# Performance work log

Hardware: AMD Instinct MI355X
Metric: run time of the kernel (lower is better)

The kernel has to match this reference:

```python
import jax, jax.numpy as jnp
import numpy as np
import math

D_MODEL = 512
N_HEADS = 8
D_HEAD = D_MODEL // N_HEADS
TEMP = math.sqrt(D_HEAD)


def setup_inputs() -> dict:
    key = jax.random.key(0)
    k1, k2, k3, k4, k5, k6 = jax.random.split(key, 6)
    B, L = 4, 2048
    q = jax.random.normal(k1, (B, L, D_MODEL), dtype=jnp.float32)
    # bool mask, True -> zero out post-softmax attention (matches torch.where branch)
    mask = jax.random.bernoulli(k2, 0.1, (B, L, L))
    in_weight = jax.random.normal(k3, (3 * D_MODEL, D_MODEL), dtype=jnp.float32) * 0.02
    in_bias = jax.random.normal(k4, (3 * D_MODEL,), dtype=jnp.float32) * 0.02
    out_w = jax.random.normal(k5, (D_MODEL, D_MODEL), dtype=jnp.float32) * 0.02
    out_b = jax.random.normal(k6, (D_MODEL,), dtype=jnp.float32) * 0.02
    return {"q": q, "mask": mask, "in_weight": in_weight, "in_bias": in_bias,
            "out_w": out_w, "out_b": out_b}


def reference(q, mask, in_weight, in_bias, out_w, out_b):
    B, L, D = q.shape
    # per-head weight slicing exactly as the torch reshape: (H, E, 3, D)
    W = in_weight.reshape(N_HEADS, D_HEAD, 3, D)
    Bv = in_bias.reshape(N_HEADS, D_HEAD, 3)
    qw, kw, vw = W[:, :, 0, :], W[:, :, 1, :], W[:, :, 2, :]  # (H, E, D)
    qb, kb, vb = Bv[:, :, 0], Bv[:, :, 1], Bv[:, :, 2]        # (H, E)
    # self-attention: k = q, v = q (forward defaults)
    Q = jnp.einsum('bld,hed->bhle', q, qw) + qb[None, :, None, :]
    K = jnp.einsum('bld,hed->bhle', q, kw) + kb[None, :, None, :]
    V = jnp.einsum('bld,hed->bhle', q, vw) + vb[None, :, None, :]
    atn = jax.nn.softmax(jnp.einsum('bhqe,bhke->bhqk', Q, K) / TEMP, axis=-1)
    # post-softmax bool masking (faithful to the original non-standard order)
    atn = jnp.where(mask[:, None, :, :], jnp.zeros((), atn.dtype), atn)
    # QUIRK of source: attention() returns V (not atn @ V); heads = concat of V
    heads = V.transpose(0, 2, 1, 3).reshape(B, L, D)  # (B, L, D_MODEL)
    outputs = heads @ out_w.T + out_b
    masks = atn.sum(axis=1)  # sum over heads -> (B, Lq, Lk)
    return outputs, masks
```

## Files before the change

kernel.cpp:

```cpp
#include <hip/hip_runtime.h>

typedef unsigned short u16;
typedef unsigned int u32;
typedef __bf16 bf16x8 __attribute__((ext_vector_type(8)));
typedef float f32x4 __attribute__((ext_vector_type(4)));

#define B_SZ 4
#define L_SZ 2048
#define D_SZ 512
#define H_SZ 8
#define E_SZ 64

#define Q_SCALE 0.18033688011112042f

#define WS_FLAG   0
#define WS_WPACK  1024
#define WS_BPACK  (WS_WPACK + 1572864)
#define WS_WOUT   (WS_BPACK + 6144)
#define WS_QBF    (WS_WOUT + 524288)
#define WS_Q      (WS_QBF + 8388608)
#define WS_K      (WS_Q + 8388608)
#define WS_V      (WS_K + 8388608)
#define WS_STATS  (WS_V + 8388608)

static __device__ __forceinline__ u16 f2bf(float f) {
  unsigned int u = __float_as_uint(f);
  u += 0x7FFFu + ((u >> 16) & 1u);
  return (u16)(u >> 16);
}

static __device__ __forceinline__ float fexp2(float x) {
  return __builtin_amdgcn_exp2f(x);
}

union FragU { bf16x8 v; uint4 u4; unsigned long long ul[2]; };

static __device__ __forceinline__ int gperm(int d) {
  int t = d & 31;
  return (d & ~31) | ((t & 12) << 1) | ((t & 16) >> 2) | (t & 3);
}

static __device__ __forceinline__ bf16x8 qfrag(const u16* __restrict__ Qp,
                                               int row, int half, int lg) {
  FragU f;
  f.u4 = *reinterpret_cast<const uint4*>(
      (const char*)Qp + (size_t)row * 128 + (half << 6) + (lg << 4));
  return f.v;
}

static __device__ __forceinline__ void gload_lds16(const void* g, void* l) {
  __builtin_amdgcn_global_load_lds(
      (const __attribute__((address_space(1))) void*)g,
      (__attribute__((address_space(3))) void*)l, 16, 0, 0);
}

static __device__ __forceinline__ void stage_k128(const u16* __restrict__ Kh, int kb0,
                                                  char* tile, int w, int lane) {
#pragma unroll
  for (int i = 0; i < 4; i++) {
    int r = w * 32 + i * 8 + (lane >> 3);
    int y = (lane & 7) << 4;
    const char* g = (const char*)Kh + (size_t)(kb0 + r) * 128 + (y ^ ((r & 7) << 4));
    gload_lds16(g, tile + w * 4096 + i * 1024);
  }
}

static __device__ __forceinline__ bf16x8 lds_frag(const char* tile, int c, int half,
                                                  int lr, int lg) {
  int r = c * 16 + lr;
  int off = ((half << 6) | (lg << 4)) ^ ((r & 7) << 4);
  FragU f;
  f.u4 = *reinterpret_cast<const uint4*>(tile + r * 128 + off);
  return f.v;
}

__global__ __launch_bounds__(256) void kdetect(const unsigned int* __restrict__ w,
                                               int* __restrict__ flag) {
  int fB = 0, fF = 0;
  for (int i = blockIdx.x * blockDim.x + threadIdx.x; i < 262144;
       i += gridDim.x * blockDim.x) {
    unsigned int v = w[i];
    if (v == 0x3F800000u) fF = 1;
    else if (v > 1u) fB = 1;
  }
  if (__any(fB)) { if ((threadIdx.x & 63) == 0) atomicOr(&flag[0], 1); }
  if (__any(fF)) { if ((threadIdx.x & 63) == 0) atomicOr(&flag[1], 1); }
}

__global__ __launch_bounds__(256) void kcast(const float* __restrict__ q,
                                             u16* __restrict__ qbf) {
  int i = blockIdx.x * blockDim.x + threadIdx.x;
  int row = i >> 6, c = i & 63;
  int g = c >> 2, lg = c & 3;
  const float* src = q + (size_t)row * 512 + g * 32 + lg * 4;
  float4 v0 = *reinterpret_cast<const float4*>(src);
  float4 v1 = *reinterpret_cast<const float4*>(src + 16);
  u32 w0 = f2bf(v0.x) | ((u32)f2bf(v0.y) << 16);
  u32 w1 = f2bf(v0.z) | ((u32)f2bf(v0.w) << 16);
  u32 w2 = f2bf(v1.x) | ((u32)f2bf(v1.y) << 16);
  u32 w3 = f2bf(v1.z) | ((u32)f2bf(v1.w) << 16);
  uint4 out = {w0, w1, w2, w3};
  *reinterpret_cast<uint4*>(qbf + (size_t)row * 512 + c * 8) = out;
}

__global__ __launch_bounds__(256) void kpack(const float* __restrict__ w_in,
                                             const float* __restrict__ b_in,
                                             const float* __restrict__ w_out,
                                             u16* __restrict__ Wpack, float* __restrict__ bpack,
                                             u16* __restrict__ Wout) {
  const int T0 = 1536 * 512;
  const int T1 = T0 + 512 * 512;
  const int T2 = T1 + 1536;
  for (int i = blockIdx.x * blockDim.x + threadIdx.x; i < T2; i += gridDim.x * blockDim.x) {
    if (i < T0) {
      int n = i >> 9, d = i & 511;
      int sel = n >> 9, idx = n & 511;
      int h = idx >> 6, e = idx & 63;
      int row = h * 192 + e * 3 + sel;
      float v = w_in[row * 512 + d];
      if (sel == 0) v *= Q_SCALE;
      Wpack[(size_t)n * 512 + gperm(d)] = f2bf(v);
    } else if (i < T1) {
      int j = i - T0;
      int n = j >> 9, d = j & 511;
      Wout[(size_t)n * 512 + gperm(d)] = f2bf(w_out[j]);
    } else {
      int n = i - T1;
      int sel = n >> 9, idx = n & 511;
      int h = idx >> 6, e = idx & 63;
      int row = h * 192 + e * 3 + sel;
      float v = b_in[row];
      if (sel == 0) v *= Q_SCALE;
      bpack[n] = v;
    }
  }
}

static __device__ __forceinline__ void stage_tile(const u16* __restrict__ A,
                                                  const u16* __restrict__ Bw,
                                                  int m0, int n0, int t,
                                                  char* tA, char* tB, int tid) {
  int w64 = tid & ~63;
#pragma unroll
  for (int i = 0; i < 4; i++) {
    int cl = tid + i * 256;
    int r = cl >> 3, c = cl & 7;
    size_t gofs = (size_t)r * 1024 + t * 128 + ((c ^ (r & 7)) << 4);
    gload_lds16((const char*)A + (size_t)m0 * 1024 + gofs, tA + (i * 256 + w64) * 16);
    gload_lds16((const char*)Bw + (size_t)n0 * 1024 + gofs, tB + (i * 256 + w64) * 16);
  }
}

template<int MODE>
__global__ __launch_bounds__(256) void kgemm(const u16* __restrict__ A,
                                             const u16* __restrict__ Bw,
                                             const float* __restrict__ bias,
                                             u16* __restrict__ Qb, u16* __restrict__ Kb,
                                             u16* __restrict__ Vb, float* __restrict__ outp) {
  __shared__ __align__(128) char tA[2][16384], tB[2][16384];
  int tid = threadIdx.x;
  int w = tid >> 6, lane = tid & 63;
  int lr = lane & 15, lg = lane >> 4;
  int m0 = blockIdx.x * 128, n0 = blockIdx.y * 128;
  int wr = w >> 1, wc = w & 1;

  f32x4 acc[4][4] = {};

  stage_tile(A, Bw, m0, n0, 0, tA[0], tB[0], tid);
  __syncthreads();
#pragma unroll 1
  for (int t = 0; t < 8; t++) {
    if (t < 7) stage_tile(A, Bw, m0, n0, t + 1, tA[(t + 1) & 1], tB[(t + 1) & 1], tid);
    const char* mA = tA[t & 1] + wr * 64 * 128;
    const char* mB = tB[t & 1] + wc * 64 * 128;
#pragma unroll
    for (int gg = 0; gg < 2; gg++) {
      bf16x8 af[4], bf_[4];
#pragma unroll
      for (int i = 0; i < 4; i++) af[i] = lds_frag(mA, i, gg, lr, lg);
#pragma unroll
      for (int j = 0; j < 4; j++) bf_[j] = lds_frag(mB, j, gg, lr, lg);
#pragma unroll
      for (int i = 0; i < 4; i++)
#pragma unroll
        for (int j = 0; j < 4; j++)
          acc[i][j] = __builtin_amdgcn_mfma_f32_16x16x32_bf16(af[i], bf_[j], acc[i][j], 0, 0, 0);
    }
    __syncthreads();
  }

#pragma unroll
  for (int j = 0; j < 4; j++) {
    int col = n0 + wc * 64 + j * 16 + lr;
    float bb = bias[col];
#pragma unroll
    for (int i = 0; i < 4; i++) {
#pragma unroll
      for (int jj = 0; jj < 4; jj++) {
        int row = m0 + wr * 64 + i * 16 + lg * 4 + jj;
        float val = acc[i][j][jj] + bb;
        if (MODE == 1) {
          outp[(size_t)row * 512 + col] = val;
        } else {
          u16 bv = f2bf(val);
          int b = row >> 11, l = row & 2047;
          if (col < 512) {
            int h = col >> 6, e = col & 63;
            Qb[((((size_t)(b * 8 + h)) << 11) + l) * 64 + gperm(e)] = bv;
          } else if (col < 1024) {
            int c2 = col - 512, h = c2 >> 6, e = c2 & 63;
            Kb[((((size_t)(b * 8 + h)) << 11) + l) * 64 + gperm(e)] = bv;
          } else {
            Vb[(size_t)row * 512 + gperm(col - 1024)] = bv;
          }
        }
      }
    }
  }
}

__global__ __launch_bounds__(256, 4) void kstats(const u16* __restrict__ Qb,
                                                 const u16* __restrict__ Kb,
                                                 float* __restrict__ stats) {
  __shared__ __align__(128) char tile[2][16384];
  int bh = blockIdx.x;
  int w = threadIdx.x >> 6, lane = threadIdx.x & 63;
  int lr = lane & 15, lg = lane >> 4;
  int q0 = blockIdx.y * 64 + w * 16;
  const u16* Qp = Qb + (size_t)bh * L_SZ * E_SZ;
  const u16* Kp = Kb + (size_t)bh * L_SZ * E_SZ;

  bf16x8 bq0 = qfrag(Qp, q0 + lr, 0, lg);
  bf16x8 bq1 = qfrag(Qp, q0 + lr, 1, lg);
  float s = 0.0f;

  stage_k128(Kp, 0, tile[0], w, lane);
  __syncthreads();
#pragma unroll 1
  for (int t = 0; t < 16; t++) {
    if (t + 1 < 16) stage_k128(Kp, (t + 1) * 128, tile[(t + 1) & 1], w, lane);
    const char* tl = tile[t & 1];
#pragma unroll 2
    for (int c = 0; c < 8; c++) {
      bf16x8 a0 = lds_frag(tl, c, 0, lr, lg);
      bf16x8 a1 = lds_frag(tl, c, 1, lr, lg);
      f32x4 d = {0.f, 0.f, 0.f, 0.f};
      d = __builtin_amdgcn_mfma_f32_16x16x32_bf16(a0, bq0, d, 0, 0, 0);
      d = __builtin_amdgcn_mfma_f32_16x16x32_bf16(a1, bq1, d, 0, 0, 0);
      s += fexp2(d[0]) + fexp2(d[1]) + fexp2(d[2]) + fexp2(d[3]);
    }
    __syncthreads();
  }
  s += __shfl_xor(s, 16);
  s += __shfl_xor(s, 32);
  if (lane < 16) stats[(size_t)bh * L_SZ + q0 + lr] = 1.0f / s;
}

__global__ __launch_bounds__(256, 4) void kmasks(const u16* __restrict__ Qb,
                                                 const u16* __restrict__ Kb,
                                                 const float* __restrict__ stats,
                                                 const void* __restrict__ mask,
                                                 const int* __restrict__ flag,
                                                 float* __restrict__ outp) {
  __shared__ __align__(128) char tile[2][16384];
  int b = blockIdx.z;
  int w = threadIdx.x >> 6, lane = threadIdx.x & 63;
  int lr = lane & 15, lg = lane >> 4;
  int q0 = blockIdx.y * 64 + w * 16;
  int kb0 = blockIdx.x * 128;
  int mode = flag[0] ? 1 : (flag[1] ? 2 : 0);

  f32x4 P[8] = {};

  stage_k128(Kb + (size_t)(b * 8) * L_SZ * E_SZ, kb0, tile[0], w, lane);
  __syncthreads();
#pragma unroll 1
  for (int h = 0; h < 8; h++) {
    if (h + 1 < 8)
      stage_k128(Kb + (size_t)(b * 8 + h + 1) * L_SZ * E_SZ, kb0, tile[(h + 1) & 1], w, lane);
    const u16* Qp = Qb + (size_t)(b * 8 + h) * L_SZ * E_SZ;
    bf16x8 bq0 = qfrag(Qp, q0 + lr, 0, lg);
    bf16x8 bq1 = qfrag(Qp, q0 + lr, 1, lg);
    float rr = stats[(size_t)(b * 8 + h) * L_SZ + q0 + lr];
    const char* tl = tile[h & 1];
#pragma unroll 2
    for (int c = 0; c < 8; c++) {
      bf16x8 a0 = lds_frag(tl, c, 0, lr, lg);
      bf16x8 a1 = lds_frag(tl, c, 1, lr, lg);
      f32x4 d = {0.f, 0.f, 0.f, 0.f};
      d = __builtin_amdgcn_mfma_f32_16x16x32_bf16(a0, bq0, d, 0, 0, 0);
      d = __builtin_amdgcn_mfma_f32_16x16x32_bf16(a1, bq1, d, 0, 0, 0);
#pragma unroll
      for (int j = 0; j < 4; j++) P[c][j] += fexp2(d[j]) * rr;
    }
    __syncthreads();
  }

  int q = q0 + lr;
  float* mrow = outp + (size_t)B_SZ * L_SZ * D_SZ
              + (size_t)b * L_SZ * L_SZ + (size_t)q * L_SZ + kb0;
  size_t moff = (size_t)b * L_SZ * L_SZ + (size_t)q * L_SZ + kb0;
#pragma unroll
  for (int c = 0; c < 8; c++) {
    int kk = c * 16 + lg * 4;
    f32x4 v = P[c];
    if (mode == 1) {
      u32 mb = *reinterpret_cast<const u32*>((const unsigned char*)mask + moff + kk);
      if ((mb      ) & 0xFF) v[0] = 0.f;
      if ((mb >>  8) & 0xFF) v[1] = 0.f;
      if ((mb >> 16) & 0xFF) v[2] = 0.f;
      if ((mb >> 24) & 0xFF) v[3] = 0.f;
    } else if (mode == 0) {
      int4 mi = *reinterpret_cast<const int4*>((const int*)mask + moff + kk);
      if (mi.x) v[0] = 0.f;
      if (mi.y) v[1] = 0.f;
      if (mi.z) v[2] = 0.f;
      if (mi.w) v[3] = 0.f;
    } else {
      float4 mf = *reinterpret_cast<const float4*>((const float*)mask + moff + kk);
      if (mf.x != 0.f) v[0] = 0.f;
      if (mf.y != 0.f) v[1] = 0.f;
      if (mf.z != 0.f) v[2] = 0.f;
      if (mf.w != 0.f) v[3] = 0.f;
    }
    *reinterpret_cast<f32x4*>(mrow + kk) = v;
  }
}

extern "C" void kernel_launch(void* const* d_in, const int* in_sizes, int n_in,
                              void* d_out, int out_size, void* d_ws, size_t ws_size,
                              hipStream_t stream) {
  (void)in_sizes; (void)n_in; (void)out_size; (void)ws_size;
  const float* q     = (const float*)d_in[0];
  const void*  mask  = d_in[1];
  const float* w_in  = (const float*)d_in[2];
  const float* b_in  = (const float*)d_in[3];
  const float* w_out = (const float*)d_in[4];
  const float* b_out = (const float*)d_in[5];
  float* outp = (float*)d_out;
  char* ws = (char*)d_ws;

  int*    flag  = (int*)(ws + WS_FLAG);
  u16*    Wpack = (u16*)(ws + WS_WPACK);
  float*  bpack = (float*)(ws + WS_BPACK);
  u16*    Wout  = (u16*)(ws + WS_WOUT);
  u16*    qbf   = (u16*)(ws + WS_QBF);
  u16*    Qb    = (u16*)(ws + WS_Q);
  u16*    Kb    = (u16*)(ws + WS_K);
  u16*    Vb    = (u16*)(ws + WS_V);
  float*  stats = (float*)(ws + WS_STATS);

  hipMemsetAsync(flag, 0, 16, stream);
  hipLaunchKernelGGL(kdetect, dim3(256), dim3(256), 0, stream, (const unsigned int*)mask, flag);
  hipLaunchKernelGGL(kcast, dim3(2048), dim3(256), 0, stream, q, qbf);
  hipLaunchKernelGGL(kpack, dim3(2048), dim3(256), 0, stream, w_in, b_in, w_out,
                     Wpack, bpack, Wout);
  hipLaunchKernelGGL((kgemm<0>), dim3(64, 12), dim3(256), 0, stream,
                     qbf, Wpack, bpack, Qb, Kb, Vb, (float*)nullptr);
  hipLaunchKernelGGL((kgemm<1>), dim3(64, 4), dim3(256), 0, stream,
                     Vb, Wout, b_out, (u16*)nullptr, (u16*)nullptr, (u16*)nullptr, outp);
  hipLaunchKernelGGL(kstats, dim3(32, 32), dim3(256), 0, stream, Qb, Kb, stats);
  hipLaunchKernelGGL(kmasks, dim3(16, 32, 4), dim3(256), 0, stream, Qb, Kb, stats, mask, flag, outp);
}
```

Measured before the change: 148.3 us.

## Load K fragments directly from global memory instead of LDS staging

Drops the double-buffered LDS staging of K tiles in both the stats and masks kernels. Each wave now reads its K fragments straight from global memory, relying on L1/L2 to serve the reuse across waves. This removes the barriers and the LDS footprint, which may raise occupancy. The masks kernel also prefetches the next head's Q fragments and row statistic into registers. The cost is redundant global and cache traffic, since four waves read the same K rows, and less control over latency hiding.

```diff
diff --git a/kernel.cpp b/kernel.cpp
--- a/kernel.cpp
+++ b/kernel.cpp
@@ -52,17 +52,6 @@
   __builtin_amdgcn_global_load_lds(
       (const __attribute__((address_space(1))) void*)g,
       (__attribute__((address_space(3))) void*)l, 16, 0, 0);
-}
-
-static __device__ __forceinline__ void stage_k128(const u16* __restrict__ Kh, int kb0,
-                                                  char* tile, int w, int lane) {
-#pragma unroll
-  for (int i = 0; i < 4; i++) {
-    int r = w * 32 + i * 8 + (lane >> 3);
-    int y = (lane & 7) << 4;
-    const char* g = (const char*)Kh + (size_t)(kb0 + r) * 128 + (y ^ ((r & 7) << 4));
-    gload_lds16(g, tile + w * 4096 + i * 1024);
-  }
 }
 
 static __device__ __forceinline__ bf16x8 lds_frag(const char* tile, int c, int half,
@@ -222,7 +211,6 @@
 __global__ __launch_bounds__(256, 4) void kstats(const u16* __restrict__ Qb,
                                                  const u16* __restrict__ Kb,
                                                  float* __restrict__ stats) {
-  __shared__ __align__(128) char tile[2][16384];
   int bh = blockIdx.x;
   int w = threadIdx.x >> 6, lane = threadIdx.x & 63;
   int lr = lane & 15, lg = lane >> 4;
@@ -234,22 +222,14 @@
   bf16x8 bq1 = qfrag(Qp, q0 + lr, 1, lg);
   float s = 0.0f;
 
-  stage_k128(Kp, 0, tile[0], w, lane);
-  __syncthreads();
-#pragma unroll 1
-  for (int t = 0; t < 16; t++) {
-    if (t + 1 < 16) stage_k128(Kp, (t + 1) * 128, tile[(t + 1) & 1], w, lane);
-    const char* tl = tile[t & 1];
-#pragma unroll 2
-    for (int c = 0; c < 8; c++) {
-      bf16x8 a0 = lds_frag(tl, c, 0, lr, lg);
-      bf16x8 a1 = lds_frag(tl, c, 1, lr, lg);
-      f32x4 d = {0.f, 0.f, 0.f, 0.f};
-      d = __builtin_amdgcn_mfma_f32_16x16x32_bf16(a0, bq0, d, 0, 0, 0);
-      d = __builtin_amdgcn_mfma_f32_16x16x32_bf16(a1, bq1, d, 0, 0, 0);
-      s += fexp2(d[0]) + fexp2(d[1]) + fexp2(d[2]) + fexp2(d[3]);
-    }
-    __syncthreads();
+#pragma unroll 8
+  for (int c = 0; c < 128; c++) {
+    bf16x8 a0 = qfrag(Kp, c * 16 + lr, 0, lg);
+    bf16x8 a1 = qfrag(Kp, c * 16 + lr, 1, lg);
+    f32x4 d = {0.f, 0.f, 0.f, 0.f};
+    d = __builtin_amdgcn_mfma_f32_16x16x32_bf16(a0, bq0, d, 0, 0, 0);
+    d = __builtin_amdgcn_mfma_f32_16x16x32_bf16(a1, bq1, d, 0, 0, 0);
+    s += fexp2(d[0]) + fexp2(d[1]) + fexp2(d[2]) + fexp2(d[3]);
   }
   s += __shfl_xor(s, 16);
   s += __shfl_xor(s, 32);
@@ -262,38 +242,40 @@
                                                  const void* __restrict__ mask,
                                                  const int* __restrict__ flag,
                                                  float* __restrict__ outp) {
-  __shared__ __align__(128) char tile[2][16384];
   int b = blockIdx.z;
   int w = threadIdx.x >> 6, lane = threadIdx.x & 63;
   int lr = lane & 15, lg = lane >> 4;
   int q0 = blockIdx.y * 64 + w * 16;
   int kb0 = blockIdx.x * 128;
   int mode = flag[0] ? 1 : (flag[1] ? 2 : 0);
+  const size_t LE = (size_t)L_SZ * E_SZ;
 
   f32x4 P[8] = {};
 
-  stage_k128(Kb + (size_t)(b * 8) * L_SZ * E_SZ, kb0, tile[0], w, lane);
-  __syncthreads();
+  bf16x8 nq0 = qfrag(Qb + (size_t)(b * 8) * LE, q0 + lr, 0, lg);
+  bf16x8 nq1 = qfrag(Qb + (size_t)(b * 8) * LE, q0 + lr, 1, lg);
+  float nrr = stats[(size_t)(b * 8) * L_SZ + q0 + lr];
 #pragma unroll 1
   for (int h = 0; h < 8; h++) {
-    if (h + 1 < 8)
-      stage_k128(Kb + (size_t)(b * 8 + h + 1) * L_SZ * E_SZ, kb0, tile[(h + 1) & 1], w, lane);
-    const u16* Qp = Qb + (size_t)(b * 8 + h) * L_SZ * E_SZ;
-    bf16x8 bq0 = qfrag(Qp, q0 + lr, 0, lg);
-    bf16x8 bq1 = qfrag(Qp, q0 + lr, 1, lg);
-    float rr = stats[(size_t)(b * 8 + h) * L_SZ + q0 + lr];
-    const char* tl = tile[h & 1];
-#pragma unroll 2
+    bf16x8 bq0 = nq0, bq1 = nq1;
+    float rr = nrr;
+    if (h + 1 < 8) {
+      const u16* Qn = Qb + (size_t)(b * 8 + h + 1) * LE;
+      nq0 = qfrag(Qn, q0 + lr, 0, lg);
+      nq1 = qfrag(Qn, q0 + lr, 1, lg);
+      nrr = stats[(size_t)(b * 8 + h + 1) * L_SZ + q0 + lr];
+    }
+    const u16* Kp = Kb + (size_t)(b * 8 + h) * LE;
+#pragma unroll
     for (int c = 0; c < 8; c++) {
-      bf16x8 a0 = lds_frag(tl, c, 0, lr, lg);
-      bf16x8 a1 = lds_frag(tl, c, 1, lr, lg);
+      bf16x8 a0 = qfrag(Kp, kb0 + c * 16 + lr, 0, lg);
+      bf16x8 a1 = qfrag(Kp, kb0 + c * 16 + lr, 1, lg);
       f32x4 d = {0.f, 0.f, 0.f, 0.f};
       d = __builtin_amdgcn_mfma_f32_16x16x32_bf16(a0, bq0, d, 0, 0, 0);
       d = __builtin_amdgcn_mfma_f32_16x16x32_bf16(a1, bq1, d, 0, 0, 0);
 #pragma unroll
       for (int j = 0; j < 4; j++) P[c][j] += fexp2(d[j]) * rr;
     }
-    __syncthreads();
   }
 
   int q = q0 + lr;
```

After: 333.6 us. 125% more time.
